# Optimization experiments

Hardware: AMD Instinct MI355X
Metric: run time of the kernel (lower is better)

Reference implementation:

```python
import jax, jax.numpy as jnp
import numpy as np

DT = 0.1
DX = 1.0
DY = 1.0
NUM_STEPS = 5
EPS = 1e-06


def _smooth3(c):
    # replicate-pad 3-tap mean filter along last axis (matches F.pad replicate + conv1d)
    cp = jnp.concatenate([c[..., :1], c, c[..., -1:]], axis=-1)
    return (cp[..., :-2] + cp[..., 1:-1] + cp[..., 2:]) / 3.0


def _thomas(a, b, c, d):
    # a, b, c, d: (M, N). Batched Thomas solve, sequential recurrence over N via lax.scan.
    M, N = d.shape
    a0 = a.at[:, 0].set(0.0)  # a[:,0] unused; zero it so the first scan step gives c0/(b0+eps)

    def fwd(carry, inp):
        c_prev, d_prev = carry
        ai, bi, ci, di = inp
        denom = bi - ai * c_prev + EPS
        cs = ci / denom
        ds = (di - ai * d_prev) / denom
        return (cs, ds), (cs, ds)

    init = (jnp.zeros((M,), d.dtype), jnp.zeros((M,), d.dtype))
    _, (c_star, d_star) = jax.lax.scan(fwd, init, (a0.T, b.T, c.T, d.T))  # (N, M)

    def bwd(x_next, inp):
        cs, ds = inp
        x = ds - cs * x_next
        return x, x

    x_last = d_star[-1]
    _, x_rest = jax.lax.scan(bwd, x_last, (c_star[:-1], d_star[:-1]), reverse=True)
    x = jnp.concatenate([x_rest, x_last[None, :]], axis=0)  # (N, M)
    return x.T


def _diffuse_rows(u2, coef2, dt, dh):
    # u2, coef2: (M, N) rows solved independently
    cs = _smooth3(coef2) * dt / (dh * dh)
    a = -cs
    c = -cs
    b = 1.0 + 2.0 * cs
    b = b.at[:, 0].set(1.0 + cs[:, 0])
    b = b.at[:, -1].set(1.0 + cs[:, -1])
    return _thomas(a, b, c, u2)


def _coef_at(base, tcoef, t):
    return jnp.clip(base + tcoef * t, EPS, None)


def _forward(u, alpha_base, beta_base, alpha_time_coeff, beta_time_coeff):
    B, C, H, W = u.shape
    t = 0.0
    for _ in range(NUM_STEPS):
        # half step in x
        alpha = _coef_at(alpha_base, alpha_time_coeff, t)  # (C,H,W)
        af = jnp.broadcast_to(alpha[None], (B, C, H, W)).reshape(B * C * H, W)
        u = _diffuse_rows(u.reshape(B * C * H, W), af, DT / 2, DX).reshape(B, C, H, W)
        t += DT / 2
        # full step in y (transpose H<->W)
        beta = _coef_at(beta_base, beta_time_coeff, t)
        ut = jnp.swapaxes(u, 2, 3).reshape(B * C * W, H)
        bf = jnp.broadcast_to(jnp.swapaxes(beta, 1, 2)[None], (B, C, W, H)).reshape(B * C * W, H)
        ut = _diffuse_rows(ut, bf, DT, DY).reshape(B, C, W, H)
        u = jnp.swapaxes(ut, 2, 3)
        t += DT / 2
        # half step in x
        alpha = _coef_at(alpha_base, alpha_time_coeff, t)
        af = jnp.broadcast_to(alpha[None], (B, C, H, W)).reshape(B * C * H, W)
        u = _diffuse_rows(u.reshape(B * C * H, W), af, DT / 2, DX).reshape(B, C, H, W)
    return u


def setup_inputs() -> dict:
    key = jax.random.key(0)
    k1, k2, k3, k4, k5 = jax.random.split(key, 5)
    B, C, S = 2048, 3, 32
    u = jax.random.normal(k1, (B, C, S, S), dtype=jnp.float32)
    alpha_base = 1.0 + 0.1 * jax.random.normal(k2, (C, S, S), dtype=jnp.float32)
    beta_base = 1.0 + 0.1 * jax.random.normal(k3, (C, S, S), dtype=jnp.float32)
    alpha_time_coeff = 0.05 * jax.random.normal(k4, (C, S, S), dtype=jnp.float32)
    beta_time_coeff = 0.05 * jax.random.normal(k5, (C, S, S), dtype=jnp.float32)
    return {"u": u, "alpha_base": alpha_base, "beta_base": beta_base,
            "alpha_time_coeff": alpha_time_coeff, "beta_time_coeff": beta_time_coeff}


def reference(u, alpha_base, beta_base, alpha_time_coeff, beta_time_coeff):
    return _forward(u, alpha_base, beta_base, alpha_time_coeff, beta_time_coeff)
```

## Files before the change

kernel.cpp:

```cpp
#include <hip/hip_runtime.h>

static constexpr float EPSF = 1e-6f;


__global__ __launch_bounds__(64) void coef_kernel(
    const float* __restrict__ alpha_base, const float* __restrict__ beta_base,
    const float* __restrict__ alpha_tc,   const float* __restrict__ beta_tc,
    float2* __restrict__ C2)
{
    int gid  = blockIdx.x * 64 + threadIdx.x;
    int pair = gid >> 5;
    int ln   = gid & 31;
    if (pair >= 33) return;
    int set = pair / 3;
    int ch  = pair % 3;
    bool isX = (set < 6);
    float t  = isX ? 0.1f * (float)set : 0.1f * (float)(set - 6) + 0.05f;
    float dt = isX ? 0.05f : 0.1f;

    const float* bp; const float* tp; int stride;
    if (isX) { bp = alpha_base + (ch * 32 + ln) * 32; tp = alpha_tc + (ch * 32 + ln) * 32; stride = 1; }
    else     { bp = beta_base  + ch * 1024 + ln;      tp = beta_tc  + ch * 1024 + ln;      stride = 32; }

    float c[32];
    #pragma unroll
    for (int i = 0; i < 32; ++i)
        c[i] = fmaxf(fmaf(tp[i * stride], t, bp[i * stride]), EPSF);

    float cs[32];
    #pragma unroll
    for (int i = 0; i < 32; ++i) {
        float l = (i == 0)  ? c[0]  : c[i - 1];
        float r = (i == 31) ? c[31] : c[i + 1];
        cs[i] = (l + c[i] + r) / 3.0f * dt;
    }

    float p[32], sn[32];
    {
        float den = (1.0f + cs[0]) + EPSF;
        p[0]  = 1.0f / den;
        sn[0] = cs[0] * p[0];
        float sprev = -sn[0];
        #pragma unroll
        for (int i = 1; i < 32; ++i) {
            float bi = (i == 31) ? (1.0f + cs[31]) : fmaf(2.0f, cs[i], 1.0f);
            float ai = -cs[i];
            float dd = (bi - ai * sprev) + EPSF;
            float pi = 1.0f / dd;
            p[i]  = pi;
            float si = ai * pi;
            sn[i] = -si;
            sprev = si;
        }
    }

    float2* o = C2 + (set * 3 + ch) * 1024 + ln;
    #pragma unroll
    for (int k = 0; k < 32; ++k) o[k * 32] = make_float2(p[k], sn[k]);
}

__device__ __forceinline__ void loadc(float p[32], float sn[32],
                                      const float2* __restrict__ c)
{
    #pragma unroll
    for (int k = 0; k < 32; ++k) { float2 v = c[k * 32]; p[k] = v.x; sn[k] = v.y; }
}

__device__ __forceinline__ void solve_reg(float d[32], const float p[32], const float sn[32])
{
    float prev = d[0] * p[0];
    d[0] = prev;
    #pragma unroll
    for (int i = 1; i < 32; ++i) {
        prev = fmaf(sn[i], prev, d[i] * p[i]);
        d[i] = prev;
    }
    #pragma unroll
    for (int i = 30; i >= 0; --i)
        d[i] = fmaf(sn[i], d[i + 1], d[i]);
}

__global__ __launch_bounds__(256, 3) void diff_kernel(
    const float* __restrict__ u_in, float* __restrict__ u_out,
    const float2* __restrict__ C2, int blocksPerCh)
{
    __shared__ float tile[8 * 1088];
    const int tid = threadIdx.x;
    const int bid = blockIdx.x;
    const int ch  = bid / blocksPerCh;
    const int b0  = (bid % blocksPerCh) * 8;
    const int wv  = tid >> 6;
    const int l   = tid & 63;
    const int ls  = tid >> 5;
    const int ln  = tid & 31;

    const float2* cb = C2 + ch * 1024 + ln;
    float p[32], sn[32];
    loadc(p, sn, cb);
    __builtin_amdgcn_sched_barrier(0);

    {
        const int sp = b0 + wv * 2;
        #pragma unroll
        for (int j = 0; j < 8; ++j) {
            int q   = j * 64 + l;
            int sl  = q >> 8;
            int rem = q & 255;
            const float4 v = reinterpret_cast<const float4*>(
                u_in + ((sp + sl) * 3 + ch) * 1024)[rem];
            float* dst = &tile[(wv * 2 + sl) * 1088 + (rem >> 3) * 34 + ((rem & 7) << 2)];
            dst[0] = v.x; dst[1] = v.y; dst[2] = v.z; dst[3] = v.w;
        }
    }

    float* tb = &tile[ls * 1088];
    float d[32];
    #pragma unroll
    for (int j = 0; j < 16; ++j) {
        float2 v = *(const float2*)(tb + ln * 34 + 2 * j);
        d[2 * j] = v.x; d[2 * j + 1] = v.y;
    }
    solve_reg(d, p, sn);

    const float2* cy = cb + 6 * 3072;
    const float2* cx = cb + 1 * 3072;

    for (int step = 0; step < 5; ++step) {
        loadc(p, sn, cy); cy += 3072;
        __builtin_amdgcn_sched_barrier(0);
        #pragma unroll
        for (int j = 0; j < 16; ++j)
            *(float2*)(tb + ln * 34 + 2 * j) = make_float2(d[2 * j], d[2 * j + 1]);
        #pragma unroll
        for (int i = 0; i < 32; ++i)
            d[i] = tb[i * 34 + ln];
        solve_reg(d, p, sn);

        loadc(p, sn, cx); cx += 3072;
        __builtin_amdgcn_sched_barrier(0);
        #pragma unroll
        for (int i = 0; i < 32; ++i)
            tb[i * 34 + ln] = d[i];
        #pragma unroll
        for (int j = 0; j < 16; ++j) {
            float2 v = *(const float2*)(tb + ln * 34 + 2 * j);
            d[2 * j] = v.x; d[2 * j + 1] = v.y;
        }
        solve_reg(d, p, sn);
        if (step < 4) solve_reg(d, p, sn);
    }

    #pragma unroll
    for (int j = 0; j < 16; ++j)
        *(float2*)(tb + ln * 34 + 2 * j) = make_float2(d[2 * j], d[2 * j + 1]);
    {
        const int sp = b0 + wv * 2;
        #pragma unroll
        for (int j = 0; j < 8; ++j) {
            int q   = j * 64 + l;
            int sl  = q >> 8;
            int rem = q & 255;
            const float* s_ = &tile[(wv * 2 + sl) * 1088 + (rem >> 3) * 34 + ((rem & 7) << 2)];
            float4 v; v.x = s_[0]; v.y = s_[1]; v.z = s_[2]; v.w = s_[3];
            reinterpret_cast<float4*>(u_out + ((sp + sl) * 3 + ch) * 1024)[rem] = v;
        }
    }
}

extern "C" void kernel_launch(void* const* d_in, const int* in_sizes, int n_in,
                              void* d_out, int out_size, void* d_ws, size_t ws_size,
                              hipStream_t stream)
{
    const float* u   = (const float*)d_in[0];
    const float* ab  = (const float*)d_in[1];
    const float* bb  = (const float*)d_in[2];
    const float* atc = (const float*)d_in[3];
    const float* btc = (const float*)d_in[4];
    float* out = (float*)d_out;
    float2* C2 = (float2*)d_ws;

    const int B = in_sizes[0] / (3 * 32 * 32);
    const int blocksPerCh = B / 8;

    coef_kernel<<<17, 64, 0, stream>>>(ab, bb, atc, btc, C2);
    diff_kernel<<<3 * blocksPerCh, 256, 0, stream>>>(u, out, C2, blocksPerCh);
}
```

Measured before the change: 118.4 us.

## Solve two batch samples per thread to reuse coefficient registers

```diff
diff --git a/kernel.cpp b/kernel.cpp
--- a/kernel.cpp
+++ b/kernel.cpp
@@ -6,7 +6,7 @@
 __global__ __launch_bounds__(64) void coef_kernel(
     const float* __restrict__ alpha_base, const float* __restrict__ beta_base,
     const float* __restrict__ alpha_tc,   const float* __restrict__ beta_tc,
-    float2* __restrict__ C2)
+    float4* __restrict__ C4)
 {
     int gid  = blockIdx.x * 64 + threadIdx.x;
     int pair = gid >> 5;
@@ -54,116 +54,135 @@
         }
     }
 
-    float2* o = C2 + (set * 3 + ch) * 1024 + ln;
-    #pragma unroll
-    for (int k = 0; k < 32; ++k) o[k * 32] = make_float2(p[k], sn[k]);
-}
-
-__device__ __forceinline__ void loadc(float p[32], float sn[32],
-                                      const float2* __restrict__ c)
-{
-    #pragma unroll
-    for (int k = 0; k < 32; ++k) { float2 v = c[k * 32]; p[k] = v.x; sn[k] = v.y; }
-}
-
-__device__ __forceinline__ void solve_reg(float d[32], const float p[32], const float sn[32])
-{
-    float prev = d[0] * p[0];
+    float4* o = C4 + (set * 3 + ch) * 512 + ln;
+    #pragma unroll
+    for (int kk = 0; kk < 16; ++kk)
+        o[kk * 32] = make_float4(p[2 * kk], sn[2 * kk], p[2 * kk + 1], sn[2 * kk + 1]);
+}
+
+__device__ __forceinline__ void loadc4(float p[32], float sn[32],
+                                       const float4* __restrict__ c)
+{
+    #pragma unroll
+    for (int kk = 0; kk < 16; ++kk) {
+        float4 v = c[kk * 32];
+        p[2 * kk]      = v.x; sn[2 * kk]     = v.y;
+        p[2 * kk + 1]  = v.z; sn[2 * kk + 1] = v.w;
+    }
+}
+
+__device__ __forceinline__ void solve2(float2 d[32], const float p[32], const float sn[32])
+{
+    float2 prev;
+    prev.x = d[0].x * p[0];
+    prev.y = d[0].y * p[0];
     d[0] = prev;
     #pragma unroll
     for (int i = 1; i < 32; ++i) {
-        prev = fmaf(sn[i], prev, d[i] * p[i]);
+        prev.x = fmaf(sn[i], prev.x, d[i].x * p[i]);
+        prev.y = fmaf(sn[i], prev.y, d[i].y * p[i]);
         d[i] = prev;
     }
     #pragma unroll
-    for (int i = 30; i >= 0; --i)
-        d[i] = fmaf(sn[i], d[i + 1], d[i]);
-}
-
-__global__ __launch_bounds__(256, 3) void diff_kernel(
+    for (int i = 30; i >= 0; --i) {
+        d[i].x = fmaf(sn[i], d[i + 1].x, d[i].x);
+        d[i].y = fmaf(sn[i], d[i + 1].y, d[i].y);
+    }
+}
+
+__global__ __launch_bounds__(128, 2) void diff_kernel(
     const float* __restrict__ u_in, float* __restrict__ u_out,
-    const float2* __restrict__ C2, int blocksPerCh)
-{
-    __shared__ float tile[8 * 1088];
+    const float4* __restrict__ C4, int blocksPerCh)
+{
+    __shared__ float4 tile4[4 * 544];
+    float2* tile2 = reinterpret_cast<float2*>(tile4);
+
     const int tid = threadIdx.x;
     const int bid = blockIdx.x;
     const int ch  = bid / blocksPerCh;
     const int b0  = (bid % blocksPerCh) * 8;
-    const int wv  = tid >> 6;
+    const int w   = tid >> 6;
     const int l   = tid & 63;
-    const int ls  = tid >> 5;
-    const int ln  = tid & 31;
-
-    const float2* cb = C2 + ch * 1024 + ln;
-    float p[32], sn[32];
-    loadc(p, sn, cb);
+    const int lp  = (w << 1) + (l >> 5);
+    const int ln  = l & 31;
+
+    const int bA = b0 + lp * 2;
+    const float4* gA = reinterpret_cast<const float4*>(u_in + (bA * 3 + ch) * 1024);
+    const float4* gB = gA + 768;
+
+    const float4* cb = C4 + ch * 512 + ln;
+    float pA[32], snA[32], pB[32], snB[32];
+    loadc4(pA, snA, cb);
     __builtin_amdgcn_sched_barrier(0);
 
-    {
-        const int sp = b0 + wv * 2;
-        #pragma unroll
-        for (int j = 0; j < 8; ++j) {
-            int q   = j * 64 + l;
-            int sl  = q >> 8;
-            int rem = q & 255;
-            const float4 v = reinterpret_cast<const float4*>(
-                u_in + ((sp + sl) * 3 + ch) * 1024)[rem];
-            float* dst = &tile[(wv * 2 + sl) * 1088 + (rem >> 3) * 34 + ((rem & 7) << 2)];
-            dst[0] = v.x; dst[1] = v.y; dst[2] = v.z; dst[3] = v.w;
+    const int srow = ln >> 3, schk = ln & 7;
+    float4* tp4 = tile4 + lp * 544;
+    float2* tp2 = tile2 + lp * 1088;
+    #pragma unroll
+    for (int r = 0; r < 8; ++r) {
+        const int row = r * 4 + srow;
+        float4 a = gA[row * 8 + schk];
+        float4 b = gB[row * 8 + schk];
+        tp4[row * 17 + 2 * schk]     = make_float4(a.x, b.x, a.y, b.y);
+        tp4[row * 17 + 2 * schk + 1] = make_float4(a.z, b.z, a.w, b.w);
+    }
+    loadc4(pB, snB, cb + 6 * 1536);
+    __builtin_amdgcn_sched_barrier(0);
+
+    float2 d[32];
+    #pragma unroll
+    for (int j = 0; j < 16; ++j) {
+        float4 v = tp4[ln * 17 + j];
+        d[2 * j]     = make_float2(v.x, v.y);
+        d[2 * j + 1] = make_float2(v.z, v.w);
+    }
+    solve2(d, pA, snA);
+
+    const float4* cx = cb + 1 * 1536;
+    const float4* cy = cb + 7 * 1536;
+
+    for (int step = 0; step < 5; ++step) {
+        loadc4(pA, snA, cx); cx += 1536;
+        __builtin_amdgcn_sched_barrier(0);
+        #pragma unroll
+        for (int j = 0; j < 16; ++j)
+            tp4[ln * 17 + j] = make_float4(d[2 * j].x, d[2 * j].y,
+                                           d[2 * j + 1].x, d[2 * j + 1].y);
+        #pragma unroll
+        for (int i = 0; i < 32; ++i)
+            d[i] = tp2[i * 34 + ln];
+        solve2(d, pB, snB);
+
+        if (step < 4) {
+            loadc4(pB, snB, cy); cy += 1536;
+            __builtin_amdgcn_sched_barrier(0);
         }
-    }
-
-    float* tb = &tile[ls * 1088];
-    float d[32];
-    #pragma unroll
-    for (int j = 0; j < 16; ++j) {
-        float2 v = *(const float2*)(tb + ln * 34 + 2 * j);
-        d[2 * j] = v.x; d[2 * j + 1] = v.y;
-    }
-    solve_reg(d, p, sn);
-
-    const float2* cy = cb + 6 * 3072;
-    const float2* cx = cb + 1 * 3072;
-
-    for (int step = 0; step < 5; ++step) {
-        loadc(p, sn, cy); cy += 3072;
-        __builtin_amdgcn_sched_barrier(0);
-        #pragma unroll
-        for (int j = 0; j < 16; ++j)
-            *(float2*)(tb + ln * 34 + 2 * j) = make_float2(d[2 * j], d[2 * j + 1]);
         #pragma unroll
         for (int i = 0; i < 32; ++i)
-            d[i] = tb[i * 34 + ln];
-        solve_reg(d, p, sn);
-
-        loadc(p, sn, cx); cx += 3072;
-        __builtin_amdgcn_sched_barrier(0);
-        #pragma unroll
-        for (int i = 0; i < 32; ++i)
-            tb[i * 34 + ln] = d[i];
+            tp2[i * 34 + ln] = d[i];
         #pragma unroll
         for (int j = 0; j < 16; ++j) {
-            float2 v = *(const float2*)(tb + ln * 34 + 2 * j);
-            d[2 * j] = v.x; d[2 * j + 1] = v.y;
+            float4 v = tp4[ln * 17 + j];
+            d[2 * j]     = make_float2(v.x, v.y);
+            d[2 * j + 1] = make_float2(v.z, v.w);
         }
-        solve_reg(d, p, sn);
-        if (step < 4) solve_reg(d, p, sn);
+        solve2(d, pA, snA);
+        if (step < 4) solve2(d, pA, snA);
     }
 
     #pragma unroll
     for (int j = 0; j < 16; ++j)
-        *(float2*)(tb + ln * 34 + 2 * j) = make_float2(d[2 * j], d[2 * j + 1]);
-    {
-        const int sp = b0 + wv * 2;
-        #pragma unroll
-        for (int j = 0; j < 8; ++j) {
-            int q   = j * 64 + l;
-            int sl  = q >> 8;
-            int rem = q & 255;
-            const float* s_ = &tile[(wv * 2 + sl) * 1088 + (rem >> 3) * 34 + ((rem & 7) << 2)];
-            float4 v; v.x = s_[0]; v.y = s_[1]; v.z = s_[2]; v.w = s_[3];
-            reinterpret_cast<float4*>(u_out + ((sp + sl) * 3 + ch) * 1024)[rem] = v;
-        }
+        tp4[ln * 17 + j] = make_float4(d[2 * j].x, d[2 * j].y,
+                                       d[2 * j + 1].x, d[2 * j + 1].y);
+    float4* oA = reinterpret_cast<float4*>(u_out + (bA * 3 + ch) * 1024);
+    float4* oB = oA + 768;
+    #pragma unroll
+    for (int r = 0; r < 8; ++r) {
+        const int row = r * 4 + srow;
+        float4 c0 = tp4[row * 17 + 2 * schk];
+        float4 c1 = tp4[row * 17 + 2 * schk + 1];
+        oA[row * 8 + schk] = make_float4(c0.x, c0.z, c1.x, c1.z);
+        oB[row * 8 + schk] = make_float4(c0.y, c0.w, c1.y, c1.w);
     }
 }
 
@@ -177,11 +196,11 @@
     const float* atc = (const float*)d_in[3];
     const float* btc = (const float*)d_in[4];
     float* out = (float*)d_out;
-    float2* C2 = (float2*)d_ws;
+    float4* C4 = (float4*)d_ws;
 
     const int B = in_sizes[0] / (3 * 32 * 32);
     const int blocksPerCh = B / 8;
 
-    coef_kernel<<<17, 64, 0, stream>>>(ab, bb, atc, btc, C2);
-    diff_kernel<<<3 * blocksPerCh, 256, 0, stream>>>(u, out, C2, blocksPerCh);
-}
+    coef_kernel<<<17, 64, 0, stream>>>(ab, bb, atc, btc, C4);
+    diff_kernel<<<3 * blocksPerCh, 128, 0, stream>>>(u, out, C4, blocksPerCh);
+}
```

Measured after the change: 165.4 us. 1.4x slower.
